# Performance work log

Hardware: AMD Instinct MI355X
Metric: run time of the kernel (lower is better)

Reference implementation:

```python
import jax, jax.numpy as jnp
import numpy as np

N_NODES = 50000
N_EDGES = 800000
NFEAT = 512
NHID = 128


def gcn_conv(x, W, b, src, dst, n_nodes):
    """PyG-style GCNConv: self-loops + symmetric deg^{-1/2} normalization."""
    # degrees over edges incl. self-loops (src/dst already contain them)
    deg = jax.ops.segment_sum(jnp.ones_like(src, dtype=x.dtype), dst,
                              num_segments=n_nodes)
    dinv = jnp.where(deg > 0, jax.lax.rsqrt(deg), 0.0)
    norm = dinv[src] * dinv[dst]            # [E+N]
    h = x @ W                               # [N, out] dense transform first (out <= in)
    msgs = h[src] * norm[:, None]           # gather + scale
    out = jax.ops.segment_sum(msgs, dst, num_segments=n_nodes)  # scatter-add
    return out + b


def setup_inputs() -> dict:
    key = jax.random.key(0)
    k1, k2, k3, k4 = jax.random.split(key, 4)
    x = jax.random.normal(k1, (N_NODES, NFEAT), dtype=jnp.float32)
    edge_index = jax.random.randint(k2, (2, N_EDGES), 0, N_NODES, dtype=jnp.int64)
    W1 = jax.random.normal(k3, (NFEAT, 2 * NHID), dtype=jnp.float32) / np.sqrt(NFEAT)
    b1 = jnp.zeros((2 * NHID,), dtype=jnp.float32)
    W2 = jax.random.normal(k4, (2 * NHID, NHID), dtype=jnp.float32) / np.sqrt(2 * NHID)
    b2 = jnp.zeros((NHID,), dtype=jnp.float32)
    return {"x": x, "edge_index": edge_index, "W1": W1, "b1": b1, "W2": W2, "b2": b2}


def reference(x, edge_index, W1, b1, W2, b2):
    n = x.shape[0]
    loop = jnp.arange(n, dtype=edge_index.dtype)
    src = jnp.concatenate([edge_index[0], loop])  # add self-loops once, reuse per layer
    dst = jnp.concatenate([edge_index[1], loop])
    h = jax.nn.relu(gcn_conv(x, W1, b1, src, dst, n))
    # dropout is identity in eval mode (reference runs in inference mode)
    out = gcn_conv(h, W2, b2, src, dst, n)
    return out
```

## Files before the change

### kernel.cpp

```cpp
#include <hip/hip_runtime.h>
#include <cstdint>
#include <cstddef>

#define NFEAT 512
#define NH1   256
#define NH2   128

#define SCAN_BLOCK 256
#define SCAN_ELEMS 4
#define SCAN_TILE  (SCAN_BLOCK * SCAN_ELEMS)

#define P_CHUNKS 128
#define HHALF    25088
#define NP       (2 * HHALF)

typedef __attribute__((ext_vector_type(8))) short short8;
typedef __attribute__((ext_vector_type(4))) float float4v;

__device__ __forceinline__ unsigned short f2bf(float f) {
    unsigned int u = __float_as_uint(f);
    u += 0x7fffu + ((u >> 16) & 1u);
    return (unsigned short)(u >> 16);
}
__device__ __forceinline__ float bf2f(unsigned short u) {
    return __uint_as_float(((unsigned int)u) << 16);
}

__device__ __forceinline__ void load_lds16(const void* g, void* l) {
    __builtin_amdgcn_global_load_lds(
        (const __attribute__((address_space(1))) void*)g,
        (__attribute__((address_space(3))) void*)l, 16, 0, 0);
}

__global__ __launch_bounds__(256) void k_hist(const int* __restrict__ dst,
                                              int* __restrict__ hist, int E, int CE) {
    __shared__ int lh[HHALF];
    const int c    = blockIdx.x >> 1;
    const int hf   = blockIdx.x & 1;
    const int base = hf * HHALF;
    for (int i = threadIdx.x; i < HHALF; i += 256) lh[i] = 0;
    __syncthreads();
    const int lo = c * CE;
    const int hi = lo + CE < E ? lo + CE : E;
    for (int e = lo + (int)threadIdx.x; e < hi; e += 256) {
        const int d = dst[e] - base;
        if ((unsigned)d < (unsigned)HHALF) atomicAdd(&lh[d], 1);
    }
    __syncthreads();
    int* outp = hist + (size_t)c * NP + base;
    for (int i = threadIdx.x; i < HHALF; i += 256) outp[i] = lh[i];
}

__global__ void k_colreduce(const int* __restrict__ hist, int* __restrict__ degi,
                            float* __restrict__ dinv, int N) {
    const int d = blockIdx.x * blockDim.x + threadIdx.x;
    if (d >= N) return;
    int s = 0;
#pragma unroll 8
    for (int c = 0; c < P_CHUNKS; ++c) s += hist[(size_t)c * NP + d];
    degi[d] = s;
    dinv[d] = rsqrtf((float)(s + 1));
}

__global__ void k_coloffs(int* __restrict__ hist, const int* __restrict__ row_start,
                          int N) {
    const int d = blockIdx.x * blockDim.x + threadIdx.x;
    if (d >= N) return;
    int run = row_start[d];
    for (int c = 0; c < P_CHUNKS; ++c) {
        int* p = &hist[(size_t)c * NP + d];
        const int t = *p;
        *p = run;
        run += t;
    }
}

__global__ __launch_bounds__(256) void k_place(const int* __restrict__ src,
                                               const int* __restrict__ dst,
                                               const int* __restrict__ hist,
                                               int* __restrict__ csr_src, int E, int CE) {
    __shared__ int lcur[HHALF];
    const int c    = blockIdx.x >> 1;
    const int hf   = blockIdx.x & 1;
    const int base = hf * HHALF;
    const int* offp = hist + (size_t)c * NP + base;
    for (int i = threadIdx.x; i < HHALF; i += 256) lcur[i] = offp[i];
    __syncthreads();
    const int lo = c * CE;
    const int hi = lo + CE < E ? lo + CE : E;
    for (int e = lo + (int)threadIdx.x; e < hi; e += 256) {
        const int d = dst[e] - base;
        if ((unsigned)d < (unsigned)HHALF) {
            const int p = atomicAdd(&lcur[d], 1);
            csr_src[p] = src[e];
        }
    }
}

__global__ __launch_bounds__(SCAN_BLOCK) void k_scan1(
    const int* __restrict__ degi, int* __restrict__ blocksums, int N) {
    __shared__ int red[SCAN_BLOCK];
    const int t = threadIdx.x;
    const int base = blockIdx.x * SCAN_TILE + t * SCAN_ELEMS;
    int s = 0;
#pragma unroll
    for (int i = 0; i < SCAN_ELEMS; ++i) {
        const int idx = base + i;
        if (idx < N) s += degi[idx];
    }
    red[t] = s;
    __syncthreads();
    for (int off = SCAN_BLOCK / 2; off > 0; off >>= 1) {
        if (t < off) red[t] += red[t + off];
        __syncthreads();
    }
    if (t == 0) blocksums[blockIdx.x] = red[0];
}

__global__ __launch_bounds__(1024) void k_scan2(
    const int* __restrict__ blocksums, int* __restrict__ blockoffs,
    int* __restrict__ row_start, int nb, int N) {
    __shared__ int sm[1024];
    const int t = threadIdx.x;
    const int v = (t < nb) ? blocksums[t] : 0;
    sm[t] = v;
    __syncthreads();
    for (int off = 1; off < 1024; off <<= 1) {
        const int x = (t >= off) ? sm[t - off] : 0;
        __syncthreads();
        sm[t] += x;
        __syncthreads();
    }
    if (t < nb) blockoffs[t] = sm[t] - v;
    if (t == 1023) row_start[N] = sm[1023];
}

__global__ __launch_bounds__(SCAN_BLOCK) void k_scan3(
    const int* __restrict__ degi, const int* __restrict__ blockoffs,
    int* __restrict__ row_start, int N) {
    __shared__ int tsum[SCAN_BLOCK];
    const int t = threadIdx.x;
    const int base = blockIdx.x * SCAN_TILE + t * SCAN_ELEMS;
    int v[SCAN_ELEMS];
    int s = 0;
#pragma unroll
    for (int i = 0; i < SCAN_ELEMS; ++i) {
        const int idx = base + i;
        v[i] = (idx < N) ? degi[idx] : 0;
        s += v[i];
    }
    tsum[t] = s;
    __syncthreads();
    for (int off = 1; off < SCAN_BLOCK; off <<= 1) {
        const int x = (t >= off) ? tsum[t - off] : 0;
        __syncthreads();
        tsum[t] += x;
        __syncthreads();
    }
    int excl = blockoffs[blockIdx.x] + tsum[t] - s;
#pragma unroll
    for (int i = 0; i < SCAN_ELEMS; ++i) {
        const int idx = base + i;
        if (idx < N) row_start[idx] = excl;
        excl += v[i];
    }
}

__global__ void k_cvt_x(const float* __restrict__ x, const float* __restrict__ dinv,
                        unsigned short* __restrict__ xb, int Nrows, int Mp) {
    int i = blockIdx.x * blockDim.x + threadIdx.x;
    int total = Mp * (NFEAT / 4);
    if (i >= total) return;
    int row = i / (NFEAT / 4);
    int q   = (i % (NFEAT / 4)) * 4;
    ushort4 o;
    if (row < Nrows) {
        const float w = dinv[row];
        const float4 v = *(const float4*)&x[(size_t)row * NFEAT + q];
        o.x = f2bf(v.x * w); o.y = f2bf(v.y * w);
        o.z = f2bf(v.z * w); o.w = f2bf(v.w * w);
    } else {
        o.x = 0; o.y = 0; o.z = 0; o.w = 0;
    }
    *(ushort4*)&xb[(size_t)row * NFEAT + q] = o;
}

__global__ void k_cvt_wt(const float* __restrict__ W, unsigned short* __restrict__ Wt,
                         int K, int Nc) {
    int i = blockIdx.x * blockDim.x + threadIdx.x;
    if (i >= K * Nc) return;
    int k = i / Nc, n = i % Nc;
    Wt[(size_t)n * K + k] = f2bf(W[(size_t)k * Nc + n]);
}

__global__ __launch_bounds__(256) void gemm_bf16(
    const unsigned short* __restrict__ A, const unsigned short* __restrict__ Bt,
    unsigned short* __restrict__ C, int N, int K) {
    __shared__ unsigned short As[128 * 32];
    __shared__ unsigned short Bs[128 * 32];
    const int t    = threadIdx.x;
    const int wave = t >> 6, lane = t & 63;
    const int row0 = blockIdx.y * 128, col0 = blockIdx.x * 128;
    const int wm = (wave >> 1) * 64, wn = (wave & 1) * 64;
    const int sr = lane >> 2;
    const int sk = (lane & 3) * 8;
    const int quad = lane >> 4, l15 = lane & 15;

    const int ca = wave * 2;
    const unsigned short* gA0 = A  + (size_t)(row0 + ca * 16 + sr) * K + sk;
    const unsigned short* gA1 = gA0 + (size_t)16 * K;
    const unsigned short* gB0 = Bt + (size_t)(col0 + ca * 16 + sr) * K + sk;
    const unsigned short* gB1 = gB0 + (size_t)16 * K;
    unsigned short* lA0 = &As[ca * 512];
    unsigned short* lA1 = &As[(ca + 1) * 512];
    unsigned short* lB0 = &Bs[ca * 512];
    unsigned short* lB1 = &Bs[(ca + 1) * 512];

    float4v acc[4][4] = {};

    for (int k0 = 0; k0 < K; k0 += 32) {
        __syncthreads();
        load_lds16(gA0 + k0, lA0);
        load_lds16(gA1 + k0, lA1);
        load_lds16(gB0 + k0, lB0);
        load_lds16(gB1 + k0, lB1);
        __syncthreads();

        short8 a[4], b[4];
#pragma unroll
        for (int i = 0; i < 4; ++i) {
            a[i] = *(const short8*)&As[(wm + i * 16 + l15) * 32 + quad * 8];
            b[i] = *(const short8*)&Bs[(wn + i * 16 + l15) * 32 + quad * 8];
        }
#pragma unroll
        for (int mt = 0; mt < 4; ++mt)
#pragma unroll
            for (int nt = 0; nt < 4; ++nt)
                acc[mt][nt] = __builtin_amdgcn_mfma_f32_16x16x32_bf16(
                    a[mt], b[nt], acc[mt][nt], 0, 0, 0);
    }

#pragma unroll
    for (int mt = 0; mt < 4; ++mt) {
#pragma unroll
        for (int nt = 0; nt < 4; ++nt) {
            const int c = col0 + wn + nt * 16 + l15;
#pragma unroll
            for (int r = 0; r < 4; ++r) {
                const int row = row0 + wm + mt * 16 + quad * 4 + r;
                C[(size_t)row * N + c] = f2bf(acc[mt][nt][r]);
            }
        }
    }
}

template <int F, bool RELU, bool OUTF32>
__global__ __launch_bounds__(256) void k_gather(
    const int* __restrict__ row_start, const int* __restrict__ csr_src,
    const float* __restrict__ dinv, const unsigned short* __restrict__ h,
    const float* __restrict__ bias, unsigned short* __restrict__ ob,
    float* __restrict__ of, int N) {
    const int gid  = blockIdx.x * blockDim.x + threadIdx.x;
    const int node = gid >> 6;
    const int lane = gid & 63;
    if (node >= N) return;

    constexpr int EL = F / 64;
    const float wd = dinv[node];
    const int jb = row_start[node];
    const int je = row_start[node + 1];
    const unsigned short* hl = h + (size_t)lane * EL;

    float acc[EL];
    {
        const unsigned short* hp = hl + (size_t)node * F;
        if (EL == 4) {
            const ushort4 v = *(const ushort4*)hp;
            acc[0] = bf2f(v.x); acc[1] = bf2f(v.y);
            acc[2] = bf2f(v.z); acc[3] = bf2f(v.w);
        } else {
            const ushort2 v = *(const ushort2*)hp;
            acc[0] = bf2f(v.x); acc[1] = bf2f(v.y);
        }
    }

    for (int j0 = jb; j0 < je; j0 += 64) {
        int jj = j0 + lane;
        if (jj >= je) jj = je - 1;
        const int myi = csr_src[jj];
        const int rem = je - j0;
        const int cnt = rem < 64 ? rem : 64;
        int i = 0;
        for (; i + 4 <= cnt; i += 4) {
            const int s0 = __shfl(myi, i + 0);
            const int s1 = __shfl(myi, i + 1);
            const int s2 = __shfl(myi, i + 2);
            const int s3 = __shfl(myi, i + 3);
            if (EL == 4) {
                const ushort4 v0 = *(const ushort4*)(hl + (size_t)s0 * F);
                const ushort4 v1 = *(const ushort4*)(hl + (size_t)s1 * F);
                const ushort4 v2 = *(const ushort4*)(hl + (size_t)s2 * F);
                const ushort4 v3 = *(const ushort4*)(hl + (size_t)s3 * F);
                acc[0] += bf2f(v0.x) + bf2f(v1.x) + bf2f(v2.x) + bf2f(v3.x);
                acc[1] += bf2f(v0.y) + bf2f(v1.y) + bf2f(v2.y) + bf2f(v3.y);
                acc[2] += bf2f(v0.z) + bf2f(v1.z) + bf2f(v2.z) + bf2f(v3.z);
                acc[3] += bf2f(v0.w) + bf2f(v1.w) + bf2f(v2.w) + bf2f(v3.w);
            } else {
                const ushort2 v0 = *(const ushort2*)(hl + (size_t)s0 * F);
                const ushort2 v1 = *(const ushort2*)(hl + (size_t)s1 * F);
                const ushort2 v2 = *(const ushort2*)(hl + (size_t)s2 * F);
                const ushort2 v3 = *(const ushort2*)(hl + (size_t)s3 * F);
                acc[0] += bf2f(v0.x) + bf2f(v1.x) + bf2f(v2.x) + bf2f(v3.x);
                acc[1] += bf2f(v0.y) + bf2f(v1.y) + bf2f(v2.y) + bf2f(v3.y);
            }
        }
        for (; i < cnt; ++i) {
            const int s = __shfl(myi, i);
            const unsigned short* hp = hl + (size_t)s * F;
            if (EL == 4) {
                const ushort4 v = *(const ushort4*)hp;
                acc[0] += bf2f(v.x); acc[1] += bf2f(v.y);
                acc[2] += bf2f(v.z); acc[3] += bf2f(v.w);
            } else {
                const ushort2 v = *(const ushort2*)hp;
                acc[0] += bf2f(v.x); acc[1] += bf2f(v.y);
            }
        }
    }

#pragma unroll
    for (int i = 0; i < EL; ++i) {
        float v = fmaf(acc[i], wd, bias[lane * EL + i]);
        if (OUTF32) {
            of[(size_t)node * F + lane * EL + i] = v;
        } else {
            if (RELU) v = fmaxf(v, 0.f);
            ob[(size_t)node * F + lane * EL + i] = f2bf(v * wd);
        }
    }
}

extern "C" void kernel_launch(void* const* d_in, const int* in_sizes, int n_in,
                              void* d_out, int out_size, void* d_ws, size_t ws_size,
                              hipStream_t stream) {
    const float* x   = (const float*)d_in[0];
    const int*   ei  = (const int*)d_in[1];
    const float* W1  = (const float*)d_in[2];
    const float* b1  = (const float*)d_in[3];
    const float* W2  = (const float*)d_in[4];
    const float* b2  = (const float*)d_in[5];
    float*       out = (float*)d_out;

    const int N = in_sizes[0] / NFEAT;
    const int E = in_sizes[1] / 2;
    const int Mp = ((N + 127) / 128) * 128;
    const int* srcp = ei;
    const int* dstp = ei + E;
    const int nScanBlocks = (N + SCAN_TILE - 1) / SCAN_TILE;
    const int CE = (E + P_CHUNKS - 1) / P_CHUNKS;

    char* wsb = (char*)d_ws;
    auto take = [&](size_t bytes) {
        char* p = wsb;
        wsb += (bytes + 255) & ~(size_t)255;
        return p;
    };
    int*   degi      = (int*)take((size_t)N * 4);
    int*   row_start = (int*)take((size_t)(N + 1) * 4);
    int*   csr_src   = (int*)take((size_t)E * 4);
    int*   blocksums = (int*)take((size_t)1024 * 4);
    int*   blockoffs = (int*)take((size_t)1024 * 4);
    float* dinv      = (float*)take((size_t)N * 4);
    unsigned short* xb  = (unsigned short*)take((size_t)Mp * NFEAT * 2);
    unsigned short* W1t = (unsigned short*)take((size_t)NH1 * NFEAT * 2);
    unsigned short* W2t = (unsigned short*)take((size_t)NH2 * NH1 * 2);
    const size_t hBytes    = (size_t)Mp * NH1 * 2;
    const size_t histBytes = (size_t)P_CHUNKS * NP * 4;
    char* big = take(histBytes > 2 * hBytes ? histBytes : 2 * hBytes);
    int*            hist = (int*)big;
    unsigned short* h    = (unsigned short*)big;
    unsigned short* h1   = (unsigned short*)(big + hBytes);
    unsigned short* h2   = xb;

    k_hist<<<P_CHUNKS * 2, 256, 0, stream>>>(dstp, hist, E, CE);
    k_colreduce<<<(N + 255) / 256, 256, 0, stream>>>(hist, degi, dinv, N);
    k_scan1<<<nScanBlocks, SCAN_BLOCK, 0, stream>>>(degi, blocksums, N);
    k_scan2<<<1, 1024, 0, stream>>>(blocksums, blockoffs, row_start, nScanBlocks, N);
    k_scan3<<<nScanBlocks, SCAN_BLOCK, 0, stream>>>(degi, blockoffs, row_start, N);
    k_coloffs<<<(N + 255) / 256, 256, 0, stream>>>(hist, row_start, N);
    k_place<<<P_CHUNKS * 2, 256, 0, stream>>>(srcp, dstp, hist, csr_src, E, CE);

    {
        int total = Mp * (NFEAT / 4);
        k_cvt_x<<<(total + 255) / 256, 256, 0, stream>>>(x, dinv, xb, N, Mp);
    }
    k_cvt_wt<<<(NFEAT * NH1 + 255) / 256, 256, 0, stream>>>(W1, W1t, NFEAT, NH1);
    k_cvt_wt<<<(NH1 * NH2 + 255) / 256, 256, 0, stream>>>(W2, W2t, NH1, NH2);

    {
        dim3 g(NH1 / 128, Mp / 128);
        gemm_bf16<<<g, 256, 0, stream>>>(xb, W1t, h, NH1, NFEAT);
    }
    {
        int total = N * 64;
        k_gather<NH1, true, false><<<(total + 255) / 256, 256, 0, stream>>>(
            row_start, csr_src, dinv, h, b1, h1, nullptr, N);
    }

    {
        dim3 g(NH2 / 128, Mp / 128);
        gemm_bf16<<<g, 256, 0, stream>>>(h1, W2t, h2, NH2, NH1);
    }
    {
        int total = N * 64;
        k_gather<NH2, false, true><<<(total + 255) / 256, 256, 0, stream>>>(
            row_start, csr_src, dinv, h2, b2, nullptr, out, N);
    }
}
```

Measured before the change: 374.0 us.

## Fuse x fp32-to-bf16 conversion and dinv scaling into first GEMM

Removes the separate pass that scaled x by dinv and converted it to a padded bf16 buffer. The first GEMM now loads fp32 x directly, scales and converts it in registers, and writes it to LDS. That GEMM uses 512-thread blocks covering all 256 output columns, so each x tile is read once. The two weight-transpose kernels are merged into one launch. This saves the write and re-read of a 50MB bf16 intermediate plus two launches, at the cost of non-async A loads with no prefetch inside the GEMM main loop.

```diff
diff --git a/kernel.cpp b/kernel.cpp
--- a/kernel.cpp
+++ b/kernel.cpp
@@ -166,31 +166,90 @@
     }
 }
 
-__global__ void k_cvt_x(const float* __restrict__ x, const float* __restrict__ dinv,
-                        unsigned short* __restrict__ xb, int Nrows, int Mp) {
-    int i = blockIdx.x * blockDim.x + threadIdx.x;
-    int total = Mp * (NFEAT / 4);
-    if (i >= total) return;
-    int row = i / (NFEAT / 4);
-    int q   = (i % (NFEAT / 4)) * 4;
-    ushort4 o;
-    if (row < Nrows) {
-        const float w = dinv[row];
-        const float4 v = *(const float4*)&x[(size_t)row * NFEAT + q];
-        o.x = f2bf(v.x * w); o.y = f2bf(v.y * w);
-        o.z = f2bf(v.z * w); o.w = f2bf(v.w * w);
-    } else {
-        o.x = 0; o.y = 0; o.z = 0; o.w = 0;
-    }
-    *(ushort4*)&xb[(size_t)row * NFEAT + q] = o;
-}
-
-__global__ void k_cvt_wt(const float* __restrict__ W, unsigned short* __restrict__ Wt,
-                         int K, int Nc) {
-    int i = blockIdx.x * blockDim.x + threadIdx.x;
-    if (i >= K * Nc) return;
-    int k = i / Nc, n = i % Nc;
-    Wt[(size_t)n * K + k] = f2bf(W[(size_t)k * Nc + n]);
+__global__ void k_cvt_w(const float* __restrict__ W1, unsigned short* __restrict__ W1t,
+                        const float* __restrict__ W2, unsigned short* __restrict__ W2t) {
+    const int i = blockIdx.x * blockDim.x + threadIdx.x;
+    const int T1 = NFEAT * NH1;
+    const int T2 = NH1 * NH2;
+    if (i < T1) {
+        const int k = i / NH1, n = i % NH1;
+        W1t[(size_t)n * NFEAT + k] = f2bf(W1[i]);
+    } else if (i < T1 + T2) {
+        const int j = i - T1;
+        const int k = j / NH2, n = j % NH2;
+        W2t[(size_t)n * NH1 + k] = f2bf(W2[j]);
+    }
+}
+
+__global__ __launch_bounds__(512) void gemm_x_fused(
+    const float* __restrict__ x, const float* __restrict__ dinv,
+    const unsigned short* __restrict__ Bt, unsigned short* __restrict__ C,
+    int Nrows, int K) {
+    __shared__ unsigned short As[128 * 32];
+    __shared__ unsigned short Bs[256 * 32];
+    const int t    = threadIdx.x;
+    const int wave = t >> 6, lane = t & 63;
+    const int row0 = blockIdx.x * 128;
+    const int quad = lane >> 4, l15 = lane & 15;
+    const int wm = (wave >> 2) * 64;
+    const int wn = (wave & 3) * 64;
+
+    const int arow = t >> 2;
+    const int ak   = (t & 3) * 8;
+    const int gr   = (row0 + arow < Nrows) ? row0 + arow : Nrows - 1;
+    const float wd = dinv[gr];
+    const float* gx = x + (size_t)gr * K + ak;
+    unsigned short* lA = &As[arow * 32 + ak];
+
+    const int brow = t >> 2;
+    const int bk   = (t & 3) * 8;
+    const unsigned short* gB0 = Bt + (size_t)brow * K + bk;
+    const unsigned short* gB1 = Bt + (size_t)(128 + brow) * K + bk;
+    unsigned short* lB0 = &Bs[wave * 512];
+    unsigned short* lB1 = &Bs[128 * 32 + wave * 512];
+
+    float4v acc[4][4] = {};
+
+    for (int k0 = 0; k0 < K; k0 += 32) {
+        __syncthreads();
+        load_lds16(gB0 + k0, lB0);
+        load_lds16(gB1 + k0, lB1);
+        const float4 v0 = *(const float4*)(gx + k0);
+        const float4 v1 = *(const float4*)(gx + k0 + 4);
+        short8 o;
+        o[0] = (short)f2bf(v0.x * wd); o[1] = (short)f2bf(v0.y * wd);
+        o[2] = (short)f2bf(v0.z * wd); o[3] = (short)f2bf(v0.w * wd);
+        o[4] = (short)f2bf(v1.x * wd); o[5] = (short)f2bf(v1.y * wd);
+        o[6] = (short)f2bf(v1.z * wd); o[7] = (short)f2bf(v1.w * wd);
+        *(short8*)lA = o;
+        __syncthreads();
+
+        short8 a[4], b[4];
+#pragma unroll
+        for (int i = 0; i < 4; ++i) {
+            a[i] = *(const short8*)&As[(wm + i * 16 + l15) * 32 + quad * 8];
+            b[i] = *(const short8*)&Bs[(wn + i * 16 + l15) * 32 + quad * 8];
+        }
+#pragma unroll
+        for (int mt = 0; mt < 4; ++mt)
+#pragma unroll
+            for (int nt = 0; nt < 4; ++nt)
+                acc[mt][nt] = __builtin_amdgcn_mfma_f32_16x16x32_bf16(
+                    a[mt], b[nt], acc[mt][nt], 0, 0, 0);
+    }
+
+#pragma unroll
+    for (int mt = 0; mt < 4; ++mt) {
+#pragma unroll
+        for (int nt = 0; nt < 4; ++nt) {
+            const int c = wn + nt * 16 + l15;
+#pragma unroll
+            for (int r = 0; r < 4; ++r) {
+                const int row = row0 + wm + mt * 16 + quad * 4 + r;
+                C[(size_t)row * NH1 + c] = f2bf(acc[mt][nt][r]);
+            }
+        }
+    }
 }
 
 __global__ __launch_bounds__(256) void gemm_bf16(
@@ -371,7 +430,7 @@
     int*   blocksums = (int*)take((size_t)1024 * 4);
     int*   blockoffs = (int*)take((size_t)1024 * 4);
     float* dinv      = (float*)take((size_t)N * 4);
-    unsigned short* xb  = (unsigned short*)take((size_t)Mp * NFEAT * 2);
+    unsigned short* h2r = (unsigned short*)take((size_t)Mp * NFEAT * 2);
     unsigned short* W1t = (unsigned short*)take((size_t)NH1 * NFEAT * 2);
     unsigned short* W2t = (unsigned short*)take((size_t)NH2 * NH1 * 2);
     const size_t hBytes    = (size_t)Mp * NH1 * 2;
@@ -380,7 +439,7 @@
     int*            hist = (int*)big;
     unsigned short* h    = (unsigned short*)big;
     unsigned short* h1   = (unsigned short*)(big + hBytes);
-    unsigned short* h2   = xb;
+    unsigned short* h2   = h2r;
 
     k_hist<<<P_CHUNKS * 2, 256, 0, stream>>>(dstp, hist, E, CE);
     k_colreduce<<<(N + 255) / 256, 256, 0, stream>>>(hist, degi, dinv, N);
@@ -391,16 +450,11 @@
     k_place<<<P_CHUNKS * 2, 256, 0, stream>>>(srcp, dstp, hist, csr_src, E, CE);
 
     {
-        int total = Mp * (NFEAT / 4);
-        k_cvt_x<<<(total + 255) / 256, 256, 0, stream>>>(x, dinv, xb, N, Mp);
-    }
-    k_cvt_wt<<<(NFEAT * NH1 + 255) / 256, 256, 0, stream>>>(W1, W1t, NFEAT, NH1);
-    k_cvt_wt<<<(NH1 * NH2 + 255) / 256, 256, 0, stream>>>(W2, W2t, NH1, NH2);
-
-    {
-        dim3 g(NH1 / 128, Mp / 128);
-        gemm_bf16<<<g, 256, 0, stream>>>(xb, W1t, h, NH1, NFEAT);
-    }
+        const int total = NFEAT * NH1 + NH1 * NH2;
+        k_cvt_w<<<(total + 255) / 256, 256, 0, stream>>>(W1, W1t, W2, W2t);
+    }
+
+    gemm_x_fused<<<Mp / 128, 512, 0, stream>>>(x, dinv, W1t, h, N, NFEAT);
     {
         int total = N * 64;
         k_gather<NH1, true, false><<<(total + 255) / 256, 256, 0, stream>>>(
```

New measurement: 346.7 us. 7.3% less time.
